# Performance work log

Measured on AMD Instinct MI355X. Metric: run time of the kernel, lower is better.

## Reference

```python
import jax, jax.numpy as jnp
import numpy as np

N_HIDDEN = 32
N_LATENT = 8
FEATS = 128


def _prelu(x, a):
    return jnp.where(x >= 0, x, a * x)


def _gru_cell(x, h, w_ih, w_hh, b_ih, b_hh):
    # PyTorch GRU gate order: r, z, n
    gi = w_ih @ x + b_ih            # (3H,)
    gh = w_hh @ h + b_hh            # (3H,)
    i_r, i_z, i_n = jnp.split(gi, 3)
    h_r, h_z, h_n = jnp.split(gh, 3)
    r = jax.nn.sigmoid(i_r + h_r)
    z = jax.nn.sigmoid(i_z + h_z)
    n = jnp.tanh(i_n + r * h_n)
    return (1.0 - z) * n + z * h


def setup_inputs() -> dict:
    key = jax.random.key(0)
    ks = jax.random.split(key, 32)
    H, L, F = N_HIDDEN, N_LATENT, FEATS
    s = 0.1
    inp = {
        "x": jax.random.normal(ks[0], (F,), dtype=jnp.float32),
        "hidden": jax.random.uniform(ks[1], (2, 1, H), dtype=jnp.float32),
        "eps": jax.random.normal(ks[2], (L,), dtype=jnp.float32),
        # GRU layer 0 (input = feats)
        "w_ih0": jax.random.normal(ks[3], (3 * H, F), dtype=jnp.float32) * s,
        "w_hh0": jax.random.normal(ks[4], (3 * H, H), dtype=jnp.float32) * s,
        "b_ih0": jax.random.normal(ks[5], (3 * H,), dtype=jnp.float32) * s,
        "b_hh0": jax.random.normal(ks[6], (3 * H,), dtype=jnp.float32) * s,
        # GRU layer 1 (input = hidden)
        "w_ih1": jax.random.normal(ks[7], (3 * H, H), dtype=jnp.float32) * s,
        "w_hh1": jax.random.normal(ks[8], (3 * H, H), dtype=jnp.float32) * s,
        "b_ih1": jax.random.normal(ks[9], (3 * H,), dtype=jnp.float32) * s,
        "b_hh1": jax.random.normal(ks[10], (3 * H,), dtype=jnp.float32) * s,
        # encoder
        "enc_w1": jax.random.normal(ks[11], (H, H), dtype=jnp.float32) * s,
        "enc_b1": jax.random.normal(ks[12], (H,), dtype=jnp.float32) * s,
        "enc_a1": jnp.float32(0.25),
        "enc_w2": jax.random.normal(ks[13], (H, H), dtype=jnp.float32) * s,
        "enc_b2": jax.random.normal(ks[14], (H,), dtype=jnp.float32) * s,
        "enc_a2": jnp.float32(0.25),
        "enc_w3": jax.random.normal(ks[15], (2 * L, H), dtype=jnp.float32) * s,
        "enc_b3": jax.random.normal(ks[16], (2 * L,), dtype=jnp.float32) * s,
        # decoder
        "dec_w1": jax.random.normal(ks[17], (H, L), dtype=jnp.float32) * s,
        "dec_b1": jax.random.normal(ks[18], (H,), dtype=jnp.float32) * s,
        "dec_a1": jnp.float32(0.25),
        "dec_w2": jax.random.normal(ks[19], (H, H), dtype=jnp.float32) * s,
        "dec_b2": jax.random.normal(ks[20], (H,), dtype=jnp.float32) * s,
        "dec_a2": jnp.float32(0.25),
        "dec_w3": jax.random.normal(ks[21], (F, H), dtype=jnp.float32) * s,
        "dec_b3": jax.random.normal(ks[22], (F,), dtype=jnp.float32) * s,
    }
    return inp


def reference(x, hidden, eps,
              w_ih0, w_hh0, b_ih0, b_hh0,
              w_ih1, w_hh1, b_ih1, b_hh1,
              enc_w1, enc_b1, enc_a1, enc_w2, enc_b2, enc_a2, enc_w3, enc_b3,
              dec_w1, dec_b1, dec_a1, dec_w2, dec_b2, dec_a2, dec_w3, dec_b3):
    # single timestep, batch 1: treat everything as vectors
    h0 = _gru_cell(x, hidden[0, 0], w_ih0, w_hh0, b_ih0, b_hh0)   # (32,)
    h1 = _gru_cell(h0, hidden[1, 0], w_ih1, w_hh1, b_ih1, b_hh1)  # (32,)
    out = h1  # top-layer GRU output

    e = _prelu(enc_w1 @ out + enc_b1, enc_a1)
    e = _prelu(enc_w2 @ e + enc_b2, enc_a2)
    encoded = enc_w3 @ e + enc_b3                                  # (16,)
    mu, logvar = encoded[:N_LATENT], encoded[N_LATENT:]
    std = jnp.exp(0.5 * logvar)
    z = mu + eps * std

    d = _prelu(dec_w1 @ z + dec_b1, dec_a1)
    d = _prelu(dec_w2 @ d + dec_b2, dec_a2)
    decoded = jax.nn.sigmoid(dec_w3 @ d + dec_b3)                  # (feats,)

    hidden_new = jnp.stack([h0, h1])[:, None, :]                   # (2,1,32)
    return decoded, mu, logvar, hidden_new
```

## Files before the change

### kernel.cpp

```cpp
#include <hip/hip_runtime.h>
#include <math.h>

#define NH 32
#define NL 8
#define NF 128

#define WSYNC() __builtin_amdgcn_wave_barrier()

template <int N4>
__device__ __forceinline__ float dotN(const float* __restrict__ w,
                                      const float* __restrict__ s) {
    const float4* w4 = (const float4*)w;
    float a0 = 0.f, a1 = 0.f, a2 = 0.f, a3 = 0.f;
#pragma unroll
    for (int i = 0; i < N4; ++i) {
        float4 a = w4[i];
        a0 = fmaf(a.x, s[4 * i + 0], a0);
        a1 = fmaf(a.y, s[4 * i + 1], a1);
        a2 = fmaf(a.z, s[4 * i + 2], a2);
        a3 = fmaf(a.w, s[4 * i + 3], a3);
    }
    return (a0 + a1) + (a2 + a3);
}

__device__ __forceinline__ float sigmoidf_(float x) {
    return 1.0f / (1.0f + __expf(-x));
}

__device__ __forceinline__ float tanhf_(float x) {
    float e = __expf(2.0f * x);
    return 1.0f - 2.0f / (e + 1.0f);
}

__device__ __forceinline__ float preluf_(float x, float a) {
    return x >= 0.0f ? x : a * x;
}

__global__ void __launch_bounds__(64)
omni_anomaly_kernel(const float* __restrict__ x,
                    const float* __restrict__ hidden,
                    const float* __restrict__ eps,
                    const float* __restrict__ w_ih0, const float* __restrict__ w_hh0,
                    const float* __restrict__ b_ih0, const float* __restrict__ b_hh0,
                    const float* __restrict__ w_ih1, const float* __restrict__ w_hh1,
                    const float* __restrict__ b_ih1, const float* __restrict__ b_hh1,
                    const float* __restrict__ enc_w1, const float* __restrict__ enc_b1,
                    const float* __restrict__ enc_a1,
                    const float* __restrict__ enc_w2, const float* __restrict__ enc_b2,
                    const float* __restrict__ enc_a2,
                    const float* __restrict__ enc_w3, const float* __restrict__ enc_b3,
                    const float* __restrict__ dec_w1, const float* __restrict__ dec_b1,
                    const float* __restrict__ dec_a1,
                    const float* __restrict__ dec_w2, const float* __restrict__ dec_b2,
                    const float* __restrict__ dec_a2,
                    const float* __restrict__ dec_w3, const float* __restrict__ dec_b3,
                    float* __restrict__ out) {
    __shared__ __align__(16) float sx[NF];
    __shared__ __align__(16) float sh0[NH];
    __shared__ __align__(16) float sh1[NH];
    __shared__ __align__(16) float gi0[3 * NH];
    __shared__ __align__(16) float gh0[3 * NH];
    __shared__ __align__(16) float gi1[3 * NH];
    __shared__ __align__(16) float gh1[3 * NH];
    __shared__ __align__(16) float h0n[NH];
    __shared__ __align__(16) float h1n[NH];
    __shared__ __align__(16) float e1b[NH];
    __shared__ __align__(16) float e2b[NH];
    __shared__ __align__(16) float eo[2 * NL];
    __shared__ __align__(16) float zb[NL];
    __shared__ __align__(16) float d1b[NH];
    __shared__ __align__(16) float d2b[NH];

    const int t = threadIdx.x;

    float h0reg = 0.f, h1reg = 0.f;
    if (t < NF / 4) {
        ((float4*)sx)[t] = ((const float4*)x)[t];
    }
    if (t < NH) {
        h0reg = hidden[t];
        h1reg = hidden[NH + t];
        sh0[t] = h0reg;
        sh1[t] = h1reg;
    }
    WSYNC();

    gi0[t] = dotN<NF / 4>(w_ih0 + t * NF, sx) + b_ih0[t];
    if (t < 32) {
        int r = 64 + t;
        gi0[r] = dotN<NF / 4>(w_ih0 + r * NF, sx) + b_ih0[r];
    } else {
        int r = 3 * (t - 32);
        gh0[r + 0] = dotN<NH / 4>(w_hh0 + (r + 0) * NH, sh0) + b_hh0[r + 0];
        gh0[r + 1] = dotN<NH / 4>(w_hh0 + (r + 1) * NH, sh0) + b_hh0[r + 1];
        gh0[r + 2] = dotN<NH / 4>(w_hh0 + (r + 2) * NH, sh0) + b_hh0[r + 2];
    }
    WSYNC();

    if (t < NH) {
        float r = sigmoidf_(gi0[t] + gh0[t]);
        float z = sigmoidf_(gi0[NH + t] + gh0[NH + t]);
        float n = tanhf_(gi0[2 * NH + t] + r * gh0[2 * NH + t]);
        float h = (1.0f - z) * n + z * h0reg;
        h0n[t] = h;
        out[NF + 2 * NL + t] = h;
    }
    WSYNC();

#pragma unroll
    for (int k = 0; k < 3; ++k) {
        int d = t + 64 * k;
        if (d < 3 * NH) {
            gi1[d] = dotN<NH / 4>(w_ih1 + d * NH, h0n) + b_ih1[d];
        } else {
            int r = d - 3 * NH;
            gh1[r] = dotN<NH / 4>(w_hh1 + r * NH, sh1) + b_hh1[r];
        }
    }
    WSYNC();

    if (t < NH) {
        float r = sigmoidf_(gi1[t] + gh1[t]);
        float z = sigmoidf_(gi1[NH + t] + gh1[NH + t]);
        float n = tanhf_(gi1[2 * NH + t] + r * gh1[2 * NH + t]);
        float h = (1.0f - z) * n + z * h1reg;
        h1n[t] = h;
        out[NF + 2 * NL + NH + t] = h;
    }
    WSYNC();

    if (t < NH) {
        float v = dotN<NH / 4>(enc_w1 + t * NH, h1n) + enc_b1[t];
        e1b[t] = preluf_(v, enc_a1[0]);
    }
    WSYNC();

    if (t < NH) {
        float v = dotN<NH / 4>(enc_w2 + t * NH, e1b) + enc_b2[t];
        e2b[t] = preluf_(v, enc_a2[0]);
    }
    WSYNC();

    if (t < 2 * NL) {
        float v = dotN<NH / 4>(enc_w3 + t * NH, e2b) + enc_b3[t];
        eo[t] = v;
        out[NF + t] = v;
    }
    WSYNC();

    if (t < NL) {
        zb[t] = eo[t] + eps[t] * __expf(0.5f * eo[NL + t]);
    }
    WSYNC();

    if (t < NH) {
        float v = dotN<NL / 4>(dec_w1 + t * NL, zb) + dec_b1[t];
        d1b[t] = preluf_(v, dec_a1[0]);
    }
    WSYNC();

    if (t < NH) {
        float v = dotN<NH / 4>(dec_w2 + t * NH, d1b) + dec_b2[t];
        d2b[t] = preluf_(v, dec_a2[0]);
    }
    WSYNC();

    {
        float v0 = dotN<NH / 4>(dec_w3 + t * NH, d2b) + dec_b3[t];
        out[t] = sigmoidf_(v0);
        int r = 64 + t;
        float v1 = dotN<NH / 4>(dec_w3 + r * NH, d2b) + dec_b3[r];
        out[r] = sigmoidf_(v1);
    }
}

extern "C" void kernel_launch(void* const* d_in, const int* in_sizes, int n_in,
                              void* d_out, int out_size, void* d_ws, size_t ws_size,
                              hipStream_t stream) {
    const float* x      = (const float*)d_in[0];
    const float* hidden = (const float*)d_in[1];
    const float* eps    = (const float*)d_in[2];
    const float* w_ih0  = (const float*)d_in[3];
    const float* w_hh0  = (const float*)d_in[4];
    const float* b_ih0  = (const float*)d_in[5];
    const float* b_hh0  = (const float*)d_in[6];
    const float* w_ih1  = (const float*)d_in[7];
    const float* w_hh1  = (const float*)d_in[8];
    const float* b_ih1  = (const float*)d_in[9];
    const float* b_hh1  = (const float*)d_in[10];
    const float* enc_w1 = (const float*)d_in[11];
    const float* enc_b1 = (const float*)d_in[12];
    const float* enc_a1 = (const float*)d_in[13];
    const float* enc_w2 = (const float*)d_in[14];
    const float* enc_b2 = (const float*)d_in[15];
    const float* enc_a2 = (const float*)d_in[16];
    const float* enc_w3 = (const float*)d_in[17];
    const float* enc_b3 = (const float*)d_in[18];
    const float* dec_w1 = (const float*)d_in[19];
    const float* dec_b1 = (const float*)d_in[20];
    const float* dec_a1 = (const float*)d_in[21];
    const float* dec_w2 = (const float*)d_in[22];
    const float* dec_b2 = (const float*)d_in[23];
    const float* dec_a2 = (const float*)d_in[24];
    const float* dec_w3 = (const float*)d_in[25];
    const float* dec_b3 = (const float*)d_in[26];
    float* out = (float*)d_out;

    omni_anomaly_kernel<<<1, 64, 0, stream>>>(
        x, hidden, eps,
        w_ih0, w_hh0, b_ih0, b_hh0,
        w_ih1, w_hh1, b_ih1, b_hh1,
        enc_w1, enc_b1, enc_a1,
        enc_w2, enc_b2, enc_a2,
        enc_w3, enc_b3,
        dec_w1, dec_b1, dec_a1,
        dec_w2, dec_b2, dec_a2,
        dec_w3, dec_b3,
        out);
}
```

Measured before the change: 12.85 us.

## Split kernel into two waves and prefetch later-layer weights into registers

Launches two wavefronts instead of one. The first wave preloads all later-stage weights (GRU layer-1 input weights, encoder and decoder matrices) into registers before the serial chain starts, so the dependent layers no longer stall on global loads. The second wave computes the GRU hidden-state products for both layers in parallel with the layer-0 input product, then prefetches the final decoder weights while the first wave runs the serial encoder/decoder chain. The chain itself uses split-K dot products combined with cross-lane shuffles. The cost is two block-wide barriers, higher register pressure, and more complex indexing.

New measurement: 12.36 us. -3.8%, faster.

```diff
diff --git a/kernel.cpp b/kernel.cpp
--- a/kernel.cpp
+++ b/kernel.cpp
@@ -7,13 +7,22 @@
 
 #define WSYNC() __builtin_amdgcn_wave_barrier()
 
-template <int N4>
-__device__ __forceinline__ float dotN(const float* __restrict__ w,
-                                      const float* __restrict__ s) {
+__device__ __forceinline__ float sigmoidf_(float x) {
+    return 1.0f / (1.0f + __expf(-x));
+}
+__device__ __forceinline__ float tanhf_(float x) {
+    float e = __expf(2.0f * x);
+    return 1.0f - 2.0f / (e + 1.0f);
+}
+__device__ __forceinline__ float preluf_(float x, float a) {
+    return x >= 0.0f ? x : a * x;
+}
+
+__device__ __forceinline__ float dotG32(const float* __restrict__ w, const float* s) {
     const float4* w4 = (const float4*)w;
     float a0 = 0.f, a1 = 0.f, a2 = 0.f, a3 = 0.f;
-#pragma unroll
-    for (int i = 0; i < N4; ++i) {
+#pragma unroll 8
+    for (int i = 0; i < 32; ++i) {
         float4 a = w4[i];
         a0 = fmaf(a.x, s[4 * i + 0], a0);
         a1 = fmaf(a.y, s[4 * i + 1], a1);
@@ -22,21 +31,35 @@
     }
     return (a0 + a1) + (a2 + a3);
 }
-
-__device__ __forceinline__ float sigmoidf_(float x) {
-    return 1.0f / (1.0f + __expf(-x));
-}
-
-__device__ __forceinline__ float tanhf_(float x) {
-    float e = __expf(2.0f * x);
-    return 1.0f - 2.0f / (e + 1.0f);
-}
-
-__device__ __forceinline__ float preluf_(float x, float a) {
-    return x >= 0.0f ? x : a * x;
-}
-
-__global__ void __launch_bounds__(64)
+__device__ __forceinline__ float dotG8(const float* __restrict__ w, const float* s) {
+    const float4* w4 = (const float4*)w;
+    float a0 = 0.f, a1 = 0.f, a2 = 0.f, a3 = 0.f;
+#pragma unroll
+    for (int i = 0; i < 8; ++i) {
+        float4 a = w4[i];
+        a0 = fmaf(a.x, s[4 * i + 0], a0);
+        a1 = fmaf(a.y, s[4 * i + 1], a1);
+        a2 = fmaf(a.z, s[4 * i + 2], a2);
+        a3 = fmaf(a.w, s[4 * i + 3], a3);
+    }
+    return (a0 + a1) + (a2 + a3);
+}
+
+template <int N4>
+__device__ __forceinline__ float dotR(const float4* w, const float* s) {
+    float a0 = 0.f, a1 = 0.f, a2 = 0.f, a3 = 0.f;
+#pragma unroll
+    for (int i = 0; i < N4; ++i) {
+        float4 a = w[i];
+        a0 = fmaf(a.x, s[4 * i + 0], a0);
+        a1 = fmaf(a.y, s[4 * i + 1], a1);
+        a2 = fmaf(a.z, s[4 * i + 2], a2);
+        a3 = fmaf(a.w, s[4 * i + 3], a3);
+    }
+    return (a0 + a1) + (a2 + a3);
+}
+
+__global__ void __launch_bounds__(128)
 omni_anomaly_kernel(const float* __restrict__ x,
                     const float* __restrict__ hidden,
                     const float* __restrict__ eps,
@@ -55,122 +78,149 @@
                     const float* __restrict__ dec_a2,
                     const float* __restrict__ dec_w3, const float* __restrict__ dec_b3,
                     float* __restrict__ out) {
-    __shared__ __align__(16) float sx[NF];
-    __shared__ __align__(16) float sh0[NH];
-    __shared__ __align__(16) float sh1[NH];
-    __shared__ __align__(16) float gi0[3 * NH];
-    __shared__ __align__(16) float gh0[3 * NH];
-    __shared__ __align__(16) float gi1[3 * NH];
-    __shared__ __align__(16) float gh1[3 * NH];
-    __shared__ __align__(16) float h0n[NH];
-    __shared__ __align__(16) float h1n[NH];
-    __shared__ __align__(16) float e1b[NH];
-    __shared__ __align__(16) float e2b[NH];
-    __shared__ __align__(16) float eo[2 * NL];
-    __shared__ __align__(16) float zb[NL];
-    __shared__ __align__(16) float d1b[NH];
-    __shared__ __align__(16) float d2b[NH];
+    __shared__ __align__(16) float sxA[NF], sxB[NF];
+    __shared__ __align__(16) float shA[2 * NH], shB[2 * NH];
+    __shared__ __align__(16) float gi0[3 * NH], gh0[3 * NH], gh1[3 * NH];
+    __shared__ __align__(16) float h0n[NH], h1n[NH];
+    __shared__ __align__(16) float e1b[NH], e2b[NH], eo[2 * NL], zb[NL];
+    __shared__ __align__(16) float d1b[NH], d2b[NH];
 
     const int t = threadIdx.x;
-
-    float h0reg = 0.f, h1reg = 0.f;
-    if (t < NF / 4) {
-        ((float4*)sx)[t] = ((const float4*)x)[t];
-    }
-    if (t < NH) {
-        h0reg = hidden[t];
-        h1reg = hidden[NH + t];
-        sh0[t] = h0reg;
-        sh1[t] = h1reg;
+    const int hr = t & 31;
+    const int half = (t >> 5) & 1;
+
+    if (t < 32) {
+        ((float4*)sxA)[t] = ((const float4*)x)[t];
+    } else if (t < 48) {
+        ((float4*)shA)[t - 32] = ((const float4*)hidden)[t - 32];
+    } else if (t >= 64 && t < 96) {
+        ((float4*)sxB)[t - 64] = ((const float4*)x)[t - 64];
+    } else if (t >= 96 && t < 112) {
+        ((float4*)shB)[t - 96] = ((const float4*)hidden)[t - 96];
     }
     WSYNC();
 
-    gi0[t] = dotN<NF / 4>(w_ih0 + t * NF, sx) + b_ih0[t];
-    if (t < 32) {
-        int r = 64 + t;
-        gi0[r] = dotN<NF / 4>(w_ih0 + r * NF, sx) + b_ih0[r];
+    float4 wih1a[8], wih1b[8];
+    float4 we1[4], we2[4], wd2[4], we3[4], wd1[2];
+    float bi1a = 0.f, bi1b = 0.f, be1 = 0.f, be2 = 0.f, be3 = 0.f;
+    float bd1 = 0.f, bd2 = 0.f, epsr = 0.f;
+    float a_e1 = 0.f, a_e2 = 0.f, a_d1 = 0.f, a_d2 = 0.f;
+    if (t < 64) {
+        const float4* r = (const float4*)(w_ih1 + t * NH);
+#pragma unroll
+        for (int i = 0; i < 8; ++i) wih1a[i] = r[i];
+        bi1a = b_ih1[t];
+        if (t < 32) {
+            const float4* r2 = (const float4*)(w_ih1 + (t + 64) * NH);
+#pragma unroll
+            for (int i = 0; i < 8; ++i) wih1b[i] = r2[i];
+            bi1b = b_ih1[t + 64];
+        }
+        const float4* p1 = (const float4*)(enc_w1 + hr * NH + half * 16);
+        const float4* p2 = (const float4*)(enc_w2 + hr * NH + half * 16);
+        const float4* p4 = (const float4*)(dec_w2 + hr * NH + half * 16);
+#pragma unroll
+        for (int i = 0; i < 4; ++i) { we1[i] = p1[i]; we2[i] = p2[i]; wd2[i] = p4[i]; }
+        if (hr < 16) {
+            const float4* p3 = (const float4*)(enc_w3 + hr * NH + half * 16);
+#pragma unroll
+            for (int i = 0; i < 4; ++i) we3[i] = p3[i];
+        }
+        if (half == 0) {
+            const float4* p5 = (const float4*)(dec_w1 + hr * NL);
+            wd1[0] = p5[0]; wd1[1] = p5[1];
+            be1 = enc_b1[hr]; be2 = enc_b2[hr];
+            bd1 = dec_b1[hr]; bd2 = dec_b2[hr];
+            if (hr < 16) be3 = enc_b3[hr];
+            if (hr < 8)  epsr = eps[hr];
+        }
+        a_e1 = enc_a1[0]; a_e2 = enc_a2[0]; a_d1 = dec_a1[0]; a_d2 = dec_a2[0];
+    }
+    __builtin_amdgcn_sched_barrier(0);
+
+    if (t < 96) {
+        const float* sxw = (t < 64) ? sxA : sxB;
+        gi0[t] = dotG32(w_ih0 + t * NF, sxw) + b_ih0[t];
     } else {
-        int r = 3 * (t - 32);
-        gh0[r + 0] = dotN<NH / 4>(w_hh0 + (r + 0) * NH, sh0) + b_hh0[r + 0];
-        gh0[r + 1] = dotN<NH / 4>(w_hh0 + (r + 1) * NH, sh0) + b_hh0[r + 1];
-        gh0[r + 2] = dotN<NH / 4>(w_hh0 + (r + 2) * NH, sh0) + b_hh0[r + 2];
-    }
-    WSYNC();
-
-    if (t < NH) {
-        float r = sigmoidf_(gi0[t] + gh0[t]);
-        float z = sigmoidf_(gi0[NH + t] + gh0[NH + t]);
-        float n = tanhf_(gi0[2 * NH + t] + r * gh0[2 * NH + t]);
-        float h = (1.0f - z) * n + z * h0reg;
-        h0n[t] = h;
-        out[NF + 2 * NL + t] = h;
-    }
-    WSYNC();
-
-#pragma unroll
-    for (int k = 0; k < 3; ++k) {
-        int d = t + 64 * k;
-        if (d < 3 * NH) {
-            gi1[d] = dotN<NH / 4>(w_ih1 + d * NH, h0n) + b_ih1[d];
-        } else {
-            int r = d - 3 * NH;
-            gh1[r] = dotN<NH / 4>(w_hh1 + r * NH, sh1) + b_hh1[r];
-        }
-    }
-    WSYNC();
-
-    if (t < NH) {
-        float r = sigmoidf_(gi1[t] + gh1[t]);
-        float z = sigmoidf_(gi1[NH + t] + gh1[NH + t]);
-        float n = tanhf_(gi1[2 * NH + t] + r * gh1[2 * NH + t]);
-        float h = (1.0f - z) * n + z * h1reg;
-        h1n[t] = h;
-        out[NF + 2 * NL + NH + t] = h;
-    }
-    WSYNC();
-
-    if (t < NH) {
-        float v = dotN<NH / 4>(enc_w1 + t * NH, h1n) + enc_b1[t];
-        e1b[t] = preluf_(v, enc_a1[0]);
-    }
-    WSYNC();
-
-    if (t < NH) {
-        float v = dotN<NH / 4>(enc_w2 + t * NH, e1b) + enc_b2[t];
-        e2b[t] = preluf_(v, enc_a2[0]);
-    }
-    WSYNC();
-
-    if (t < 2 * NL) {
-        float v = dotN<NH / 4>(enc_w3 + t * NH, e2b) + enc_b3[t];
-        eo[t] = v;
-        out[NF + t] = v;
-    }
-    WSYNC();
-
-    if (t < NL) {
-        zb[t] = eo[t] + eps[t] * __expf(0.5f * eo[NL + t]);
-    }
-    WSYNC();
-
-    if (t < NH) {
-        float v = dotN<NL / 4>(dec_w1 + t * NL, zb) + dec_b1[t];
-        d1b[t] = preluf_(v, dec_a1[0]);
-    }
-    WSYNC();
-
-    if (t < NH) {
-        float v = dotN<NH / 4>(dec_w2 + t * NH, d1b) + dec_b2[t];
-        d2b[t] = preluf_(v, dec_a2[0]);
-    }
-    WSYNC();
-
-    {
-        float v0 = dotN<NH / 4>(dec_w3 + t * NH, d2b) + dec_b3[t];
-        out[t] = sigmoidf_(v0);
-        int r = 64 + t;
-        float v1 = dotN<NH / 4>(dec_w3 + r * NH, d2b) + dec_b3[r];
-        out[r] = sigmoidf_(v1);
+        int q3 = 3 * (t - 96);
+#pragma unroll
+        for (int j = 0; j < 3; ++j) {
+            gh0[q3 + j] = dotG8(w_hh0 + (q3 + j) * NH, shB) + b_hh0[q3 + j];
+            gh1[q3 + j] = dotG8(w_hh1 + (q3 + j) * NH, shB + NH) + b_hh1[q3 + j];
+        }
+    }
+    __syncthreads();
+
+    if (t < 64) {
+        if (t < 32) {
+            float r = sigmoidf_(gi0[t] + gh0[t]);
+            float z = sigmoidf_(gi0[NH + t] + gh0[NH + t]);
+            float n = tanhf_(gi0[2 * NH + t] + r * gh0[2 * NH + t]);
+            float h = (1.f - z) * n + z * shA[t];
+            h0n[t] = h;
+            out[NF + 2 * NL + t] = h;
+        }
+        WSYNC();
+        float g1a = dotR<8>(wih1a, h0n) + bi1a;
+        float g1b = 0.f;
+        if (t < 32) g1b = dotR<8>(wih1b, h0n) + bi1b;
+        int src = (t + 32) & 63;
+        float zg = __shfl(g1a, src, 64);
+        if (t < 32) {
+            float r = sigmoidf_(g1a + gh1[t]);
+            float z = sigmoidf_(zg + gh1[NH + t]);
+            float n = tanhf_(g1b + r * gh1[2 * NH + t]);
+            float h = (1.f - z) * n + z * shA[NH + t];
+            h1n[t] = h;
+            out[NF + 2 * NL + NH + t] = h;
+        }
+        WSYNC();
+        float p = dotR<4>(we1, h1n + half * 16);
+        p += __shfl_xor(p, 32, 64);
+        if (half == 0) e1b[hr] = preluf_(p + be1, a_e1);
+        WSYNC();
+        float p2v = dotR<4>(we2, e1b + half * 16);
+        p2v += __shfl_xor(p2v, 32, 64);
+        if (half == 0) e2b[hr] = preluf_(p2v + be2, a_e2);
+        WSYNC();
+        float p3v = dotR<4>(we3, e2b + half * 16);
+        p3v += __shfl_xor(p3v, 32, 64);
+        if (half == 0 && hr < 16) {
+            float v = p3v + be3;
+            eo[hr] = v;
+            out[NF + hr] = v;
+        }
+        WSYNC();
+        if (t < 8) zb[t] = eo[t] + epsr * __expf(0.5f * eo[NL + t]);
+        WSYNC();
+        if (half == 0) {
+            float v = dotR<2>(wd1, zb) + bd1;
+            d1b[hr] = preluf_(v, a_d1);
+        }
+        WSYNC();
+        float p4v = dotR<4>(wd2, d1b + half * 16);
+        p4v += __shfl_xor(p4v, 32, 64);
+        if (half == 0) d2b[hr] = preluf_(p4v + bd2, a_d2);
+    } else {
+    }
+    float4 wd3a[8], wd3b[8];
+    float bd3a = 0.f, bd3b = 0.f;
+    if (t >= 64) {
+        int q = t - 64;
+        const float4* p = (const float4*)(dec_w3 + q * NH);
+        const float4* p2 = (const float4*)(dec_w3 + (q + 64) * NH);
+#pragma unroll
+        for (int i = 0; i < 8; ++i) { wd3a[i] = p[i]; wd3b[i] = p2[i]; }
+        bd3a = dec_b3[q]; bd3b = dec_b3[q + 64];
+    }
+    __syncthreads();
+
+    if (t >= 64) {
+        int q = t - 64;
+        float v0 = dotR<8>(wd3a, d2b) + bd3a;
+        float v1 = dotR<8>(wd3b, d2b) + bd3b;
+        out[q] = sigmoidf_(v0);
+        out[q + 64] = sigmoidf_(v1);
     }
 }
 
@@ -206,7 +256,7 @@
     const float* dec_b3 = (const float*)d_in[26];
     float* out = (float*)d_out;
 
-    omni_anomaly_kernel<<<1, 64, 0, stream>>>(
+    omni_anomaly_kernel<<<1, 128, 0, stream>>>(
         x, hidden, eps,
         w_ih0, w_hh0, b_ih0, b_hh0,
         w_ih1, w_hh1, b_ih1, b_hh1,
```

## Use two waves per block and hoist layer-1 hidden GEMV into first stage

Applied to the files above, without the earlier changes.

Launches 128 threads (two wavefronts) instead of one, so the 96 input-gate rows of layer 0 each get their own thread. The recurrent GEMVs for both GRU layers are computed together in the first stage, since they depend only on the initial hidden state. Scalar PReLU slopes and eps are loaded up front, and the mu/logvar stage is fused with the reparameterisation. The price is replacing cheap wave barriers with real __syncthreads across two waves at every stage of a long serial chain.

New measurement: 12.48 us. 1.03x faster.

```diff
diff --git a/kernel.cpp b/kernel.cpp
--- a/kernel.cpp
+++ b/kernel.cpp
@@ -4,8 +4,6 @@
 #define NH 32
 #define NL 8
 #define NF 128
-
-#define WSYNC() __builtin_amdgcn_wave_barrier()
 
 template <int N4>
 __device__ __forceinline__ float dotN(const float* __restrict__ w,
@@ -26,17 +24,15 @@
 __device__ __forceinline__ float sigmoidf_(float x) {
     return 1.0f / (1.0f + __expf(-x));
 }
-
 __device__ __forceinline__ float tanhf_(float x) {
     float e = __expf(2.0f * x);
     return 1.0f - 2.0f / (e + 1.0f);
 }
-
 __device__ __forceinline__ float preluf_(float x, float a) {
     return x >= 0.0f ? x : a * x;
 }
 
-__global__ void __launch_bounds__(64)
+__global__ void __launch_bounds__(128)
 omni_anomaly_kernel(const float* __restrict__ x,
                     const float* __restrict__ hidden,
                     const float* __restrict__ eps,
@@ -56,121 +52,101 @@
                     const float* __restrict__ dec_w3, const float* __restrict__ dec_b3,
                     float* __restrict__ out) {
     __shared__ __align__(16) float sx[NF];
-    __shared__ __align__(16) float sh0[NH];
-    __shared__ __align__(16) float sh1[NH];
-    __shared__ __align__(16) float gi0[3 * NH];
-    __shared__ __align__(16) float gh0[3 * NH];
-    __shared__ __align__(16) float gi1[3 * NH];
-    __shared__ __align__(16) float gh1[3 * NH];
-    __shared__ __align__(16) float h0n[NH];
-    __shared__ __align__(16) float h1n[NH];
-    __shared__ __align__(16) float e1b[NH];
-    __shared__ __align__(16) float e2b[NH];
-    __shared__ __align__(16) float eo[2 * NL];
-    __shared__ __align__(16) float zb[NL];
-    __shared__ __align__(16) float d1b[NH];
-    __shared__ __align__(16) float d2b[NH];
+    __shared__ __align__(16) float sh[2 * NH];
+    __shared__ __align__(16) float gi0[3 * NH], gh0[3 * NH];
+    __shared__ __align__(16) float gi1[3 * NH], gh1[3 * NH];
+    __shared__ __align__(16) float h0n[NH], h1n[NH];
+    __shared__ __align__(16) float e1b[NH], e2b[NH], zb[NL];
+    __shared__ __align__(16) float d1b[NH], d2b[NH];
 
     const int t = threadIdx.x;
 
-    float h0reg = 0.f, h1reg = 0.f;
-    if (t < NF / 4) {
+    if (t < 32) {
         ((float4*)sx)[t] = ((const float4*)x)[t];
+    } else if (t < 48) {
+        ((float4*)sh)[t - 32] = ((const float4*)hidden)[t - 32];
     }
-    if (t < NH) {
-        h0reg = hidden[t];
-        h1reg = hidden[NH + t];
-        sh0[t] = h0reg;
-        sh1[t] = h1reg;
+    float a_e1 = 0.f, a_e2 = 0.f, a_d1 = 0.f, a_d2 = 0.f, epsr = 0.f;
+    if (t < 32) {
+        a_e1 = enc_a1[0]; a_e2 = enc_a2[0];
+        a_d1 = dec_a1[0]; a_d2 = dec_a2[0];
+        if (t < NL) epsr = eps[t];
     }
-    WSYNC();
+    __syncthreads();
 
-    gi0[t] = dotN<NF / 4>(w_ih0 + t * NF, sx) + b_ih0[t];
-    if (t < 32) {
-        int r = 64 + t;
-        gi0[r] = dotN<NF / 4>(w_ih0 + r * NF, sx) + b_ih0[r];
+    if (t < 96) {
+        gi0[t] = dotN<NF / 4>(w_ih0 + t * NF, sx) + b_ih0[t];
     } else {
-        int r = 3 * (t - 32);
-        gh0[r + 0] = dotN<NH / 4>(w_hh0 + (r + 0) * NH, sh0) + b_hh0[r + 0];
-        gh0[r + 1] = dotN<NH / 4>(w_hh0 + (r + 1) * NH, sh0) + b_hh0[r + 1];
-        gh0[r + 2] = dotN<NH / 4>(w_hh0 + (r + 2) * NH, sh0) + b_hh0[r + 2];
+        int q = 3 * (t - 96);
+#pragma unroll
+        for (int j = 0; j < 3; ++j) {
+            gh0[q + j] = dotN<NH / 4>(w_hh0 + (q + j) * NH, sh) + b_hh0[q + j];
+            gh1[q + j] = dotN<NH / 4>(w_hh1 + (q + j) * NH, sh + NH) + b_hh1[q + j];
+        }
     }
-    WSYNC();
+    __syncthreads();
 
     if (t < NH) {
         float r = sigmoidf_(gi0[t] + gh0[t]);
         float z = sigmoidf_(gi0[NH + t] + gh0[NH + t]);
         float n = tanhf_(gi0[2 * NH + t] + r * gh0[2 * NH + t]);
-        float h = (1.0f - z) * n + z * h0reg;
+        float h = (1.0f - z) * n + z * sh[t];
         h0n[t] = h;
         out[NF + 2 * NL + t] = h;
     }
-    WSYNC();
+    __syncthreads();
 
-#pragma unroll
-    for (int k = 0; k < 3; ++k) {
-        int d = t + 64 * k;
-        if (d < 3 * NH) {
-            gi1[d] = dotN<NH / 4>(w_ih1 + d * NH, h0n) + b_ih1[d];
-        } else {
-            int r = d - 3 * NH;
-            gh1[r] = dotN<NH / 4>(w_hh1 + r * NH, sh1) + b_hh1[r];
-        }
+    if (t < 96) {
+        gi1[t] = dotN<NH / 4>(w_ih1 + t * NH, h0n) + b_ih1[t];
     }
-    WSYNC();
+    __syncthreads();
 
     if (t < NH) {
         float r = sigmoidf_(gi1[t] + gh1[t]);
         float z = sigmoidf_(gi1[NH + t] + gh1[NH + t]);
         float n = tanhf_(gi1[2 * NH + t] + r * gh1[2 * NH + t]);
-        float h = (1.0f - z) * n + z * h1reg;
+        float h = (1.0f - z) * n + z * sh[NH + t];
         h1n[t] = h;
         out[NF + 2 * NL + NH + t] = h;
     }
-    WSYNC();
+    __syncthreads();
 
     if (t < NH) {
         float v = dotN<NH / 4>(enc_w1 + t * NH, h1n) + enc_b1[t];
-        e1b[t] = preluf_(v, enc_a1[0]);
+        e1b[t] = preluf_(v, a_e1);
     }
-    WSYNC();
+    __syncthreads();
 
     if (t < NH) {
         float v = dotN<NH / 4>(enc_w2 + t * NH, e1b) + enc_b2[t];
-        e2b[t] = preluf_(v, enc_a2[0]);
+        e2b[t] = preluf_(v, a_e2);
     }
-    WSYNC();
-
-    if (t < 2 * NL) {
-        float v = dotN<NH / 4>(enc_w3 + t * NH, e2b) + enc_b3[t];
-        eo[t] = v;
-        out[NF + t] = v;
-    }
-    WSYNC();
+    __syncthreads();
 
     if (t < NL) {
-        zb[t] = eo[t] + eps[t] * __expf(0.5f * eo[NL + t]);
+        float mu = dotN<NH / 4>(enc_w3 + t * NH, e2b) + enc_b3[t];
+        float lv = dotN<NH / 4>(enc_w3 + (NL + t) * NH, e2b) + enc_b3[NL + t];
+        out[NF + t] = mu;
+        out[NF + NL + t] = lv;
+        zb[t] = mu + epsr * __expf(0.5f * lv);
     }
-    WSYNC();
+    __syncthreads();
 
     if (t < NH) {
         float v = dotN<NL / 4>(dec_w1 + t * NL, zb) + dec_b1[t];
-        d1b[t] = preluf_(v, dec_a1[0]);
+        d1b[t] = preluf_(v, a_d1);
     }
-    WSYNC();
+    __syncthreads();
 
     if (t < NH) {
         float v = dotN<NH / 4>(dec_w2 + t * NH, d1b) + dec_b2[t];
-        d2b[t] = preluf_(v, dec_a2[0]);
+        d2b[t] = preluf_(v, a_d2);
     }
-    WSYNC();
+    __syncthreads();
 
     {
-        float v0 = dotN<NH / 4>(dec_w3 + t * NH, d2b) + dec_b3[t];
-        out[t] = sigmoidf_(v0);
-        int r = 64 + t;
-        float v1 = dotN<NH / 4>(dec_w3 + r * NH, d2b) + dec_b3[r];
-        out[r] = sigmoidf_(v1);
+        float v = dotN<NH / 4>(dec_w3 + t * NH, d2b) + dec_b3[t];
+        out[t] = sigmoidf_(v);
     }
 }
 
@@ -206,7 +182,7 @@
     const float* dec_b3 = (const float*)d_in[26];
     float* out = (float*)d_out;
 
-    omni_anomaly_kernel<<<1, 64, 0, stream>>>(
+    omni_anomaly_kernel<<<1, 128, 0, stream>>>(
         x, hidden, eps,
         w_ih0, w_hh0, b_ih0, b_hh0,
         w_ih1, w_hh1, b_ih1, b_hh1,
```
